# Optimization experiments

Measured on AMD Instinct MI355X. Metric: run time of the kernel, lower is better.

## Reference

```python
import jax, jax.numpy as jnp
import numpy as np

DIM = 1536
NHEADS = 12
HEADDIM = DIM // NHEADS  # 128
F, H, W = 5, 26, 30
S = F * H * W  # 3900
MAXPOS = 1024
EPS = 1e-6


def setup_inputs() -> dict:
    key = jax.random.key(0)
    ks = jax.random.split(key, 6)
    x = jax.random.normal(ks[0], (1, S, DIM), jnp.float32)
    seq_lens = jnp.array([S], jnp.int32)
    grid_sizes = jnp.array([[F, H, W]], jnp.int32)
    # complex RoPE table as (cos, sin) pairs: [1024, head_dim//2, 2]
    c = HEADDIM // 2
    inv = 1.0 / (10000.0 ** (np.arange(c, dtype=np.float64) / c))
    theta = np.arange(MAXPOS, dtype=np.float64)[:, None] * inv[None, :]
    freqs = jnp.asarray(np.stack([np.cos(theta), np.sin(theta)], axis=-1), jnp.float32)
    scale = 1.0 / np.sqrt(DIM)
    Wq = jax.random.normal(ks[1], (DIM, DIM), jnp.float32) * scale
    Wk = jax.random.normal(ks[2], (DIM, DIM), jnp.float32) * scale
    Wv = jax.random.normal(ks[3], (DIM, DIM), jnp.float32) * scale
    Wo = jax.random.normal(ks[4], (DIM, DIM), jnp.float32) * scale
    bq = jnp.zeros((DIM,), jnp.float32)
    bk = jnp.zeros((DIM,), jnp.float32)
    bv = jnp.zeros((DIM,), jnp.float32)
    bo = jnp.zeros((DIM,), jnp.float32)
    gq = jnp.ones((DIM,), jnp.float32)
    gk = jnp.ones((DIM,), jnp.float32)
    return dict(x=x, seq_lens=seq_lens, grid_sizes=grid_sizes, freqs=freqs,
                Wq=Wq, bq=bq, Wk=Wk, bk=bk, Wv=Wv, bv=bv, Wo=Wo, bo=bo, gq=gq, gk=gk)


def _rms_norm(z, g):
    zf = z.astype(jnp.float32)
    y = zf * jax.lax.rsqrt(jnp.mean(zf * zf, axis=-1, keepdims=True) + EPS)
    return y.astype(z.dtype) * g


def _build_freqs_i(freqs_c, f, h, w):
    # freqs_c: complex [1024, c]; split c into [c-2*(c//3), c//3, c//3] for (F,H,W)
    c = freqs_c.shape[1]
    c3 = c // 3
    c0 = c - 2 * c3
    ff = jnp.broadcast_to(freqs_c[:f, :c0][:, None, None, :], (f, h, w, c0))
    fh = jnp.broadcast_to(freqs_c[:h, c0:c0 + c3][None, :, None, :], (f, h, w, c3))
    fw = jnp.broadcast_to(freqs_c[:w, c0 + c3:][None, None, :, :], (f, h, w, c3))
    return jnp.concatenate([ff, fh, fw], axis=-1).reshape(f * h * w, 1, c)


def _rope_apply(t, freqs_i):
    # t: [1, S, n, d]; interpret last dim as c complex pairs and rotate
    b, s, n, d = t.shape
    c = d // 2
    t2 = t[0].reshape(s, n, c, 2)
    tc = jax.lax.complex(t2[..., 0], t2[..., 1])  # [S, n, c]
    tc = tc * freqs_i  # broadcast [S, 1, c]
    out = jnp.stack([jnp.real(tc), jnp.imag(tc)], axis=-1).reshape(s, n, d)
    return out[None].astype(jnp.float32)


def reference(x, seq_lens, grid_sizes, freqs, Wq, bq, Wk, bk, Wv, bv, Wo, bo, gq, gk):
    b, s, dim = x.shape
    d = freqs.shape[1] * 2  # head_dim
    n = dim // d
    q = _rms_norm(x @ Wq + bq, gq).reshape(b, s, n, d)
    k = _rms_norm(x @ Wk + bk, gk).reshape(b, s, n, d)
    v = (x @ Wv + bv).reshape(b, s, n, d)
    f, h, w = [int(t) for t in np.asarray(grid_sizes)[0]]
    freqs_c = jax.lax.complex(freqs[..., 0], freqs[..., 1])  # [1024, c]
    freqs_i = _build_freqs_i(freqs_c, f, h, w)  # [S, 1, c]
    q = _rope_apply(q, freqs_i)
    k = _rope_apply(k, freqs_i)
    # scaled dot-product attention with key-length mask
    scale = 1.0 / jnp.sqrt(jnp.asarray(d, jnp.float32))
    scores = jnp.einsum('bqnd,bknd->bnqk', q, k) * scale  # [1, n, S, S]
    key_mask = (jnp.arange(s)[None, None, None, :] < seq_lens[:, None, None, None])
    scores = jnp.where(key_mask, scores, jnp.asarray(-1e30, scores.dtype))
    attn = jax.nn.softmax(scores, axis=-1)
    out = jnp.einsum('bnqk,bknd->bqnd', attn, v)  # [1, S, n, d]
    out = out.reshape(b, s, dim)
    return out @ Wo + bo
```

## Files before the change

### kernel.cpp

```cpp
#include <hip/hip_runtime.h>
#include <stdint.h>

#define DIM 1536
#define SLEN 3900
#define SPAD 3904
#define NH 12
#define HD 128
#define SKP 136
#define SVP 68

typedef __bf16 bf16x8 __attribute__((ext_vector_type(8)));
typedef float f32x4 __attribute__((ext_vector_type(4)));

__device__ __forceinline__ float b2f(uint16_t u) {
  union { uint32_t i; float f; } x; x.i = ((uint32_t)u) << 16; return x.f;
}
__device__ __forceinline__ uint16_t f2b(float f) {
  union { float f; uint32_t i; } x; x.f = f;
  uint32_t r = (x.i + 0x7fffu + ((x.i >> 16) & 1u)) >> 16;
  return (uint16_t)r;
}
__device__ __forceinline__ bf16x8 ld8bf(const uint16_t* p) {
  bf16x8 r; __builtin_memcpy(&r, p, 16); return r;
}
__device__ __forceinline__ void st8(uint16_t* p, bf16x8 v) {
  __builtin_memcpy(p, &v, 16);
}
__device__ __forceinline__ void gl_lds16(const void* g, void* l) {
  __builtin_amdgcn_global_load_lds((__attribute__((address_space(1))) void*)(g),
                                   (__attribute__((address_space(3))) void*)(l),
                                   16, 0, 0);
}

__global__ __launch_bounds__(256) void conv_x(
    const float* __restrict__ x, uint16_t* __restrict__ xb) {
  int i = (blockIdx.x * 256 + threadIdx.x) * 8;
  float a[8];
  __builtin_memcpy(a, x + i, 32);
  uint16_t t[8];
#pragma unroll
  for (int q = 0; q < 8; q++) t[q] = f2b(a[q]);
  __builtin_memcpy(xb + i, t, 16);
}

__global__ __launch_bounds__(256) void transposeW4(
    const float* __restrict__ w0, const float* __restrict__ w1,
    const float* __restrict__ w2, const float* __restrict__ w3,
    uint16_t* __restrict__ WT4) {
  __shared__ uint16_t t[32][33];
  const int z = blockIdx.z;
  const float* src = z == 0 ? w0 : z == 1 ? w1 : z == 2 ? w2 : w3;
  uint16_t* dst = WT4 + (size_t)z * DIM * DIM;
  const int bx = blockIdx.x * 32, by = blockIdx.y * 32;
  const int tx = threadIdx.x & 31, ty = threadIdx.x >> 5;
#pragma unroll
  for (int i = 0; i < 32; i += 8)
    t[ty + i][tx] = f2b(src[(size_t)(by + ty + i) * DIM + bx + tx]);
  __syncthreads();
#pragma unroll
  for (int i = 0; i < 32; i += 8)
    dst[(size_t)(bx + ty + i) * DIM + by + tx] = t[tx][ty + i];
}

__global__ __launch_bounds__(256) void gemm(
    const uint16_t* __restrict__ A, const uint16_t* __restrict__ BT4,
    uint16_t* __restrict__ Cb, float* __restrict__ Cf,
    const float* __restrict__ bias, int M, int mode) {
  __shared__ __align__(16) uint16_t sA[128 * 32];
  __shared__ __align__(16) uint16_t sB[128 * 32];
  const int z = blockIdx.z;
  const uint16_t* BT = BT4 + (size_t)z * DIM * DIM;
  const int m0 = blockIdx.x * 128;
  const int n0 = blockIdx.y * 128;
  const int tid = threadIdx.x;
  const int wave = tid >> 6, lane = tid & 63;
  const int mh = (wave >> 1) * 64, nh = (wave & 1) * 64;
  const int lr = lane >> 2, lc = (lane & 3) * 8;
  const int r0 = wave * 32;
  const int fm = mh + (lane & 15);
  const int fn = nh + (lane & 15);
  const int ko = (lane >> 4) * 8;

  f32x4 acc[4][4];
  const f32x4 z4 = {0.f, 0.f, 0.f, 0.f};
#pragma unroll
  for (int i = 0; i < 4; i++)
#pragma unroll
    for (int j = 0; j < 4; j++) acc[i][j] = z4;

  for (int k0 = 0; k0 < DIM; k0 += 32) {
    __syncthreads();
#pragma unroll
    for (int j = 0; j < 2; j++) {
      int ra = m0 + r0 + j * 16 + lr; ra = ra < M ? ra : M - 1;
      gl_lds16(A + (size_t)ra * DIM + k0 + lc, (char*)sA + (r0 + j * 16) * 64);
      int rb = n0 + r0 + j * 16 + lr;
      gl_lds16(BT + (size_t)rb * DIM + k0 + lc, (char*)sB + (r0 + j * 16) * 64);
    }
    __builtin_amdgcn_s_waitcnt(0x0f70);
    __syncthreads();
    bf16x8 fa[4], fb[4];
#pragma unroll
    for (int i = 0; i < 4; i++) {
      fa[i] = ld8bf(sA + (fm + i * 16) * 32 + ko);
      fb[i] = ld8bf(sB + (fn + i * 16) * 32 + ko);
    }
#pragma unroll
    for (int i = 0; i < 4; i++)
#pragma unroll
      for (int j = 0; j < 4; j++)
        acc[i][j] = __builtin_amdgcn_mfma_f32_16x16x32_bf16(fa[i], fb[j], acc[i][j], 0, 0, 0);
  }
#pragma unroll
  for (int j = 0; j < 4; j++) {
    int col = n0 + nh + j * 16 + (lane & 15);
    float bvv = (mode == 0 && bias) ? bias[col] : 0.f;
#pragma unroll
    for (int i = 0; i < 4; i++) {
      int row = m0 + mh + i * 16 + (lane >> 4) * 4;
#pragma unroll
      for (int r = 0; r < 4; r++) {
        if (row + r < M) {
          float val = acc[i][j][r] + bvv;
          if (mode == 0)
            Cf[(size_t)(row + r) * DIM + col] = val;
          else
            Cb[(size_t)z * ((size_t)NH * SLEN * HD) +
               (size_t)(col >> 7) * ((size_t)SLEN * HD) +
               (size_t)(row + r) * HD + (col & 127)] = f2b(val);
        }
      }
    }
  }
}

__global__ __launch_bounds__(256) void norm_rope(
    uint16_t* __restrict__ Qb, uint16_t* __restrict__ Kb,
    const float* __restrict__ bq, const float* __restrict__ bk,
    const float* __restrict__ gq, const float* __restrict__ gk,
    const float* __restrict__ freqs, const int* __restrict__ gsz) {
  const int s = blockIdx.x;
  const int isK = blockIdx.y;
  uint32_t* B = (uint32_t*)(isK ? Kb : Qb);
  const float2* br = (const float2*)(isK ? bk : bq);
  const float2* gr = (const float2*)(isK ? gk : gq);
  const int tid = threadIdx.x;
  float va[3], vb[3];
  float ss = 0.f;
#pragma unroll
  for (int i = 0; i < 3; i++) {
    int p = tid + i * 256;
    int h = p >> 6, j = p & 63;
    size_t a = (size_t)h * (SLEN * 64) + (size_t)s * 64 + j;
    uint32_t u = B[a];
    float2 ub = br[p];
    float x0 = b2f((uint16_t)(u & 0xffff)) + ub.x;
    float x1 = b2f((uint16_t)(u >> 16)) + ub.y;
    va[i] = x0; vb[i] = x1; ss += x0 * x0 + x1 * x1;
  }
#pragma unroll
  for (int o = 32; o > 0; o >>= 1) ss += __shfl_down(ss, o, 64);
  __shared__ float red[4];
  if ((tid & 63) == 0) red[tid >> 6] = ss;
  __syncthreads();
  ss = red[0] + red[1] + red[2] + red[3];
  const float rr = rsqrtf(ss * (1.0f / DIM) + 1e-6f);
  const int H = gsz[1], W = gsz[2];
  const int hw = H * W;
  const int fi = s / hw, rem = s - fi * hw;
  const int hi = rem / W, wi = rem - hi * W;
#pragma unroll
  for (int i = 0; i < 3; i++) {
    int p = tid + i * 256;
    int h = p >> 6, j = p & 63;
    int prow = (j < 22) ? fi : (j < 43) ? hi : wi;
    float2 f2 = ((const float2*)freqs)[prow * 64 + j];
    float2 g2 = gr[p];
    float na = va[i] * rr * g2.x;
    float nb = vb[i] * rr * g2.y;
    float ra = na * f2.x - nb * f2.y;
    float rb = na * f2.y + nb * f2.x;
    size_t a = (size_t)h * (SLEN * 64) + (size_t)s * 64 + j;
    B[a] = (uint32_t)f2b(ra) | ((uint32_t)f2b(rb) << 16);
  }
}

__global__ __launch_bounds__(256) void v_reformat(
    const uint16_t* __restrict__ Vb, const float* __restrict__ bv,
    uint16_t* __restrict__ VT) {
  __shared__ uint16_t t[128][136];
  const int head = blockIdx.x;
  const int s0 = blockIdx.y * 128;
  const int tid = threadIdx.x;
  const int cb = (tid & 15) * 8, rb = tid >> 4;
  const uint16_t* Vh = Vb + (size_t)head * SLEN * HD;
  float bvf[8];
#pragma unroll
  for (int q = 0; q < 8; q++) bvf[q] = bv[head * HD + cb + q];
#pragma unroll
  for (int pass = 0; pass < 8; pass++) {
    int r = rb + pass * 16;
    int s = s0 + r; int sc = s < SLEN ? s : SLEN - 1;
    uint16_t u[8];
    __builtin_memcpy(u, Vh + (size_t)sc * HD + cb, 16);
#pragma unroll
    for (int q = 0; q < 8; q++) t[r][cb + q] = f2b(b2f(u[q]) + bvf[q]);
  }
  __syncthreads();
  const int sb = (tid & 15) * 8, db = tid >> 4;
#pragma unroll
  for (int pass = 0; pass < 8; pass++) {
    int d = db + pass * 16;
    uint16_t out[8] __attribute__((aligned(16)));
#pragma unroll
    for (int i2 = 0; i2 < 8; i2++) {
      int s = s0 + sb + i2;
      out[i2] = (s < SLEN) ? t[sb + i2][d] : (uint16_t)0;
    }
    size_t base = ((size_t)head * HD + d) * SPAD + s0 + sb;
    if (s0 + sb + 8 <= SLEN) {
      __builtin_memcpy(VT + base, out, 16);
    } else {
#pragma unroll
      for (int i2 = 0; i2 < 8; i2++) {
        int s = s0 + sb + i2;
        if (s < SPAD) VT[base + i2] = out[i2];
      }
    }
  }
}

__global__ __launch_bounds__(256) void attn(
    const uint16_t* __restrict__ Q, const uint16_t* __restrict__ K,
    const uint16_t* __restrict__ VT, uint16_t* __restrict__ O,
    const int* __restrict__ seq_lens) {
  __shared__ __align__(16) uint16_t sK[64 * SKP];
  __shared__ __align__(16) uint16_t sV[128 * SVP];
  __shared__ __align__(16) uint16_t sP[64 * SVP];
  const int head = blockIdx.x;
  const int q0 = blockIdx.y * 64;
  const int tid = threadIdx.x;
  const int wave = tid >> 6, lane = tid & 63;
  int sl = seq_lens[0];
  const int seqlen = sl < SLEN ? sl : SLEN;
  const uint16_t* Qh = Q + (size_t)head * SLEN * HD;
  const uint16_t* Kh = K + (size_t)head * SLEN * HD;
  const uint16_t* Vh = VT + (size_t)head * HD * SPAD;

  const int fm = lane & 15;
  const int ko = (lane >> 4) * 8;

#pragma unroll
  for (int ps = 0; ps < 4; ps++) {
    int idx = tid + ps * 256;
    int row = idx >> 4, cc = (idx & 15) * 8;
    int qg = q0 + row; qg = qg < SLEN ? qg : SLEN - 1;
    st8(sK + row * SKP + cc, ld8bf(Qh + (size_t)qg * HD + cc));
  }
  __syncthreads();
  bf16x8 aq[4];
#pragma unroll
  for (int kc = 0; kc < 4; kc++)
    aq[kc] = ld8bf(sK + (wave * 16 + fm) * SKP + kc * 32 + ko);

  f32x4 o[8];
  const f32x4 z4 = {0.f, 0.f, 0.f, 0.f};
#pragma unroll
  for (int j = 0; j < 8; j++) o[j] = z4;
  float l_r[4] = {0.f, 0.f, 0.f, 0.f};

  const float C1 = 0.08838834764831845f * 1.4426950408889634f;
  const float C2 = 12.0f * 1.4426950408889634f;

  for (int kv0 = 0; kv0 < SLEN; kv0 += 64) {
    __syncthreads();
#pragma unroll
    for (int ps = 0; ps < 4; ps++) {
      int idx = tid + ps * 256;
      int row = idx >> 4, cc = (idx & 15) * 8;
      int kg = kv0 + row; kg = kg < SLEN ? kg : SLEN - 1;
      st8(sK + row * SKP + cc, ld8bf(Kh + (size_t)kg * HD + cc));
    }
#pragma unroll
    for (int ps = 0; ps < 4; ps++) {
      int idx = tid + ps * 256;
      int d = idx >> 3, cc = (idx & 7) * 8;
      st8(sV + d * SVP + cc, ld8bf(Vh + (size_t)d * SPAD + kv0 + cc));
    }
    __syncthreads();

    f32x4 sc[4];
#pragma unroll
    for (int kk = 0; kk < 4; kk++) sc[kk] = z4;
#pragma unroll
    for (int kc = 0; kc < 4; kc++) {
#pragma unroll
      for (int kk = 0; kk < 4; kk++) {
        bf16x8 bkf = ld8bf(sK + (kk * 16 + fm) * SKP + kc * 32 + ko);
        sc[kk] = __builtin_amdgcn_mfma_f32_16x16x32_bf16(aq[kc], bkf, sc[kk], 0, 0, 0);
      }
    }
#pragma unroll
    for (int kk = 0; kk < 4; kk++) {
      int col = kv0 + kk * 16 + fm;
      bool valid = col < seqlen;
#pragma unroll
      for (int r = 0; r < 4; r++) {
        float p = valid ? exp2f(sc[kk][r] * C1 - C2) : 0.f;
        l_r[r] += p;
        sP[(wave * 16 + (lane >> 4) * 4 + r) * SVP + kk * 16 + fm] = f2b(p);
      }
    }
    __syncthreads();
#pragma unroll
    for (int kc = 0; kc < 2; kc++) {
      bf16x8 ap = ld8bf(sP + (wave * 16 + fm) * SVP + kc * 32 + ko);
#pragma unroll
      for (int j = 0; j < 8; j++) {
        bf16x8 bvf = ld8bf(sV + (j * 16 + fm) * SVP + kc * 32 + ko);
        o[j] = __builtin_amdgcn_mfma_f32_16x16x32_bf16(ap, bvf, o[j], 0, 0, 0);
      }
    }
  }
#pragma unroll
  for (int r = 0; r < 4; r++) {
#pragma unroll
    for (int off = 1; off < 16; off <<= 1) l_r[r] += __shfl_xor(l_r[r], off, 64);
  }
#pragma unroll
  for (int r = 0; r < 4; r++) {
    int row = q0 + wave * 16 + (lane >> 4) * 4 + r;
    if (row < SLEN) {
      float inv = 1.0f / l_r[r];
#pragma unroll
      for (int j = 0; j < 8; j++) {
        int col = head * HD + j * 16 + fm;
        O[(size_t)row * DIM + col] = f2b(o[j][r] * inv);
      }
    }
  }
}

extern "C" void kernel_launch(void* const* d_in, const int* in_sizes, int n_in,
                              void* d_out, int out_size, void* d_ws, size_t ws_size,
                              hipStream_t stream) {
  const float* x      = (const float*)d_in[0];
  const int* seq_lens = (const int*)d_in[1];
  const int* gsz      = (const int*)d_in[2];
  const float* freqs  = (const float*)d_in[3];
  const float* Wq     = (const float*)d_in[4];
  const float* bq     = (const float*)d_in[5];
  const float* Wk     = (const float*)d_in[6];
  const float* bk     = (const float*)d_in[7];
  const float* Wv     = (const float*)d_in[8];
  const float* bv     = (const float*)d_in[9];
  const float* Wo     = (const float*)d_in[10];
  const float* bo     = (const float*)d_in[11];
  const float* gq     = (const float*)d_in[12];
  const float* gk     = (const float*)d_in[13];

  char* p = (char*)d_ws;
  uint16_t* WT4 = (uint16_t*)p; p += (size_t)4 * DIM * DIM * 2;
  uint16_t* Qb  = (uint16_t*)p; p += (size_t)NH * SLEN * HD * 2;
  uint16_t* Kb  = (uint16_t*)p; p += (size_t)NH * SLEN * HD * 2;
  uint16_t* Vb  = (uint16_t*)p; p += (size_t)NH * SLEN * HD * 2;
  uint16_t* VTb = (uint16_t*)p; p += (size_t)NH * HD * SPAD * 2;
  uint16_t* xb  = VTb;
  uint16_t* AO  = Vb;

  conv_x<<<dim3(2925), 256, 0, stream>>>(x, xb);
  transposeW4<<<dim3(48, 48, 4), 256, 0, stream>>>(Wq, Wk, Wv, Wo, WT4);

  gemm<<<dim3(31, 12, 3), 256, 0, stream>>>(xb, WT4, Qb, nullptr, nullptr, SLEN, 1);

  norm_rope<<<dim3(SLEN, 2), 256, 0, stream>>>(Qb, Kb, bq, bk, gq, gk, freqs, gsz);
  v_reformat<<<dim3(NH, 31), 256, 0, stream>>>(Vb, bv, VTb);
  attn<<<dim3(NH, 61), 256, 0, stream>>>(Qb, Kb, VTb, AO, seq_lens);

  gemm<<<dim3(31, 12, 1), 256, 0, stream>>>(AO, WT4 + (size_t)3 * DIM * DIM,
                                            nullptr, (float*)d_out, bo, SLEN, 0);
}
```

Baseline: 542.8 us.

## Prefetch next K/V tile into registers and drop redundant P barrier in attention

The attention loop now issues the global loads for the next K and V tile into registers right after the LDS barrier, so those loads overlap the current tile's MFMA and softmax work. It also removes the __syncthreads between writing and reading the P tile, since each wave only touches its own 16 rows. It raises wave priority around the MFMA blocks with s_setprio and replaces the manual float-to-bf16 rounding with the native conversion. The cost is higher register pressure from the eight prefetch vectors, which could lower occupancy.

```diff
diff --git a/kernel.cpp b/kernel.cpp
--- a/kernel.cpp
+++ b/kernel.cpp
@@ -16,9 +16,7 @@
   union { uint32_t i; float f; } x; x.i = ((uint32_t)u) << 16; return x.f;
 }
 __device__ __forceinline__ uint16_t f2b(float f) {
-  union { float f; uint32_t i; } x; x.f = f;
-  uint32_t r = (x.i + 0x7fffu + ((x.i >> 16) & 1u)) >> 16;
-  return (uint16_t)r;
+  union { __bf16 h; uint16_t u; } c; c.h = (__bf16)f; return c.u;
 }
 __device__ __forceinline__ bf16x8 ld8bf(const uint16_t* p) {
   bf16x8 r; __builtin_memcpy(&r, p, 16); return r;
@@ -249,13 +247,14 @@
 
   const int fm = lane & 15;
   const int ko = (lane >> 4) * 8;
+  const int kr0 = tid >> 4, kcc = (tid & 15) * 8;
+  const int vd0 = tid >> 3, vcc = (tid & 7) * 8;
 
 #pragma unroll
   for (int ps = 0; ps < 4; ps++) {
-    int idx = tid + ps * 256;
-    int row = idx >> 4, cc = (idx & 15) * 8;
+    int row = kr0 + ps * 16;
     int qg = q0 + row; qg = qg < SLEN ? qg : SLEN - 1;
-    st8(sK + row * SKP + cc, ld8bf(Qh + (size_t)qg * HD + cc));
+    st8(sK + row * SKP + kcc, ld8bf(Qh + (size_t)qg * HD + kcc));
   }
   __syncthreads();
   bf16x8 aq[4];
@@ -272,26 +271,35 @@
   const float C1 = 0.08838834764831845f * 1.4426950408889634f;
   const float C2 = 12.0f * 1.4426950408889634f;
 
+  bf16x8 kr[4], vr[4];
+#pragma unroll
+  for (int ps = 0; ps < 4; ps++) {
+    kr[ps] = ld8bf(Kh + (size_t)(kr0 + ps * 16) * HD + kcc);
+    vr[ps] = ld8bf(Vh + (size_t)(vd0 + ps * 32) * SPAD + vcc);
+  }
+
   for (int kv0 = 0; kv0 < SLEN; kv0 += 64) {
     __syncthreads();
 #pragma unroll
     for (int ps = 0; ps < 4; ps++) {
-      int idx = tid + ps * 256;
-      int row = idx >> 4, cc = (idx & 15) * 8;
-      int kg = kv0 + row; kg = kg < SLEN ? kg : SLEN - 1;
-      st8(sK + row * SKP + cc, ld8bf(Kh + (size_t)kg * HD + cc));
-    }
-#pragma unroll
-    for (int ps = 0; ps < 4; ps++) {
-      int idx = tid + ps * 256;
-      int d = idx >> 3, cc = (idx & 7) * 8;
-      st8(sV + d * SVP + cc, ld8bf(Vh + (size_t)d * SPAD + kv0 + cc));
+      st8(sK + (kr0 + ps * 16) * SKP + kcc, kr[ps]);
+      st8(sV + (vd0 + ps * 32) * SVP + vcc, vr[ps]);
     }
     __syncthreads();
+    int nv0 = kv0 + 64;
+    if (nv0 < SLEN) {
+#pragma unroll
+      for (int ps = 0; ps < 4; ps++) {
+        int kg = nv0 + kr0 + ps * 16; kg = kg < SLEN ? kg : SLEN - 1;
+        kr[ps] = ld8bf(Kh + (size_t)kg * HD + kcc);
+        vr[ps] = ld8bf(Vh + (size_t)(vd0 + ps * 32) * SPAD + nv0 + vcc);
+      }
+    }
 
     f32x4 sc[4];
 #pragma unroll
     for (int kk = 0; kk < 4; kk++) sc[kk] = z4;
+    __builtin_amdgcn_s_setprio(1);
 #pragma unroll
     for (int kc = 0; kc < 4; kc++) {
 #pragma unroll
@@ -300,6 +308,7 @@
         sc[kk] = __builtin_amdgcn_mfma_f32_16x16x32_bf16(aq[kc], bkf, sc[kk], 0, 0, 0);
       }
     }
+    __builtin_amdgcn_s_setprio(0);
 #pragma unroll
     for (int kk = 0; kk < 4; kk++) {
       int col = kv0 + kk * 16 + fm;
@@ -311,7 +320,7 @@
         sP[(wave * 16 + (lane >> 4) * 4 + r) * SVP + kk * 16 + fm] = f2b(p);
       }
     }
-    __syncthreads();
+    __builtin_amdgcn_s_setprio(1);
 #pragma unroll
     for (int kc = 0; kc < 2; kc++) {
       bf16x8 ap = ld8bf(sP + (wave * 16 + fm) * SVP + kc * 32 + ko);
@@ -321,6 +330,7 @@
         o[j] = __builtin_amdgcn_mfma_f32_16x16x32_bf16(ap, bvf, o[j], 0, 0, 0);
       }
     }
+    __builtin_amdgcn_s_setprio(0);
   }
 #pragma unroll
   for (int r = 0; r < 4; r++) {
```

Result: faster. 469.5 us (-13.5%).
